# Performance work log

Hardware: AMD Instinct MI355X
Metric: run time of the kernel (lower is better)

## Reference

```python
import jax, jax.numpy as jnp
import numpy as np

N_NODES = 100000
N_RELS = 4
N_EDGES = 200000
D_IN = 256
D_OUT = 256
N_BASES = 2
LN_EPS = 1e-5


def setup_inputs() -> dict:
    key = jax.random.key(0)
    ks = jax.random.split(key, 8)
    x = jax.random.normal(ks[0], (N_NODES, D_IN), dtype=jnp.float32)
    src_idx = jax.random.randint(ks[1], (N_RELS, N_EDGES), 0, N_NODES, dtype=jnp.int32)
    dst_idx = jax.random.randint(ks[2], (N_RELS, N_EDGES), 0, N_NODES, dtype=jnp.int32)
    # WeightBasis: bases [B, in, out], per-relation coefficients [R, B]
    xav = float(np.sqrt(2.0)) * float(np.sqrt(6.0 / (D_IN + D_OUT)))
    bases = jax.random.uniform(ks[3], (N_BASES, D_IN, D_OUT), minval=-xav, maxval=xav, dtype=jnp.float32)
    w_comp = jax.random.normal(ks[4], (N_RELS, N_BASES), dtype=jnp.float32) * 0.5
    loop_weight = jax.random.uniform(ks[5], (D_IN, D_OUT), minval=-xav, maxval=xav, dtype=jnp.float32)
    h_bias = jnp.zeros((D_OUT,), dtype=jnp.float32)
    ln_gamma = jnp.ones((D_OUT,), dtype=jnp.float32)
    ln_beta = jnp.zeros((D_OUT,), dtype=jnp.float32)
    return {"x": x, "src_idx": src_idx, "dst_idx": dst_idx, "bases": bases,
            "w_comp": w_comp, "loop_weight": loop_weight, "h_bias": h_bias,
            "ln_gamma": ln_gamma, "ln_beta": ln_beta}


def reference(x, src_idx, dst_idx, bases, w_comp, loop_weight, h_bias, ln_gamma, ln_beta):
    n = x.shape[0]
    # basis combination -> per-relation weights [R, in, out]
    W = jnp.einsum('rb,bio->rio', w_comp, bases)

    def per_rel(W_r, s, d):
        # GraphConv(norm='right', weight=W_r): aggregate src feats to dst,
        # normalize by in-degree (clamped to 1), then matmul.
        msgs = x[s]                                            # [E, in]
        agg = jax.ops.segment_sum(msgs, d, num_segments=n)     # [N, in]
        deg = jax.ops.segment_sum(jnp.ones(d.shape, x.dtype), d, num_segments=n)
        agg = agg / jnp.maximum(deg, 1.0)[:, None]
        return agg @ W_r                                        # [N, out]

    hs = jax.vmap(per_rel)(W, src_idx, dst_idx).sum(axis=0)    # HeteroGraphConv sum aggregate
    # self-loop + bias
    h = hs + x @ loop_weight + h_bias
    # layer norm
    mu = jnp.mean(h, axis=-1, keepdims=True)
    var = jnp.mean(jnp.square(h - mu), axis=-1, keepdims=True)
    h = (h - mu) * jax.lax.rsqrt(var + LN_EPS) * ln_gamma + ln_beta
    # activation (dropout inactive in eval; NGNN has 0 layers)
    return jax.nn.relu(h)
```

## Files before the change

kernel.cpp:

```cpp
#include <hip/hip_runtime.h>


#define NN 100000
#define NR 4
#define NE 200000
#define BM 128

typedef __attribute__((ext_vector_type(8))) short short8;
typedef __attribute__((ext_vector_type(16))) float floatx16;

__device__ __forceinline__ unsigned short f2bf(float f) {
  unsigned u = __float_as_uint(f);
  u += 0x7FFFu + ((u >> 16) & 1u);
  return (unsigned short)(u >> 16);
}

__device__ __forceinline__ void gload16(const unsigned short* g, unsigned short* l) {
  __builtin_amdgcn_global_load_lds(
      (const __attribute__((address_space(1))) unsigned int*)g,
      (__attribute__((address_space(3))) unsigned int*)l, 16, 0, 0);
}

__global__ void prep(const float* __restrict__ x, const float* __restrict__ bases,
                     const float* __restrict__ loop_w, const int* __restrict__ src,
                     const int* __restrict__ dst, unsigned short* __restrict__ Xbf,
                     unsigned short* __restrict__ Bfrag, int* __restrict__ rec,
                     int* __restrict__ ovf) {
  const int b = blockIdx.x;
  const int tid = threadIdx.x;
  if (b < 3125) {
    int i = b * 256 + tid;
    int r = i / NE;
    int s = __builtin_nontemporal_load(src + i);
    int dd = __builtin_nontemporal_load(dst + i);
    int pos = atomicAdd(&rec[dd * 16], 1);
    int v = s | (r << 20);
    if (pos < 15) rec[dd * 16 + 1 + pos] = v;
    else if (pos < 31) ovf[dd * 16 + (pos - 15)] = v;
  } else if (b < 3893) {
    int i = (b - 3125) * 256 + tid;
    int e = i & 7;
    int lane = (i >> 3) & 63;
    int f = i >> 9;
    int t = f & 7;
    int j = (f >> 3) & 7;
    int s = f >> 6;
    int n = t * 32 + (lane & 31);
    int k = s * 128 + j * 16 + (lane >> 5) * 8 + e;
    float v;
    if (k < 256)      v = bases[k * 256 + n];
    else if (k < 512) v = bases[65536 + (k - 256) * 256 + n];
    else              v = loop_w[(k - 512) * 256 + n];
    Bfrag[i] = f2bf(v);
  } else {
    int i = (b - 3893) * 256 + tid;
    int row = i >> 5;
    int col = (i & 31) << 3;
    const float4 v0 = *(const float4*)(x + (size_t)row * 256 + col);
    const float4 v1 = *(const float4*)(x + (size_t)row * 256 + col + 4);
    uint4 u;
    u.x = (unsigned)f2bf(v0.x) | ((unsigned)f2bf(v0.y) << 16);
    u.y = (unsigned)f2bf(v0.z) | ((unsigned)f2bf(v0.w) << 16);
    u.z = (unsigned)f2bf(v1.x) | ((unsigned)f2bf(v1.y) << 16);
    u.w = (unsigned)f2bf(v1.z) | ((unsigned)f2bf(v1.w) << 16);
    *(uint4*)(Xbf + (size_t)row * 256 + col) = u;
  }
}

__global__ void agg_edges(const int* __restrict__ rec, const int* __restrict__ ovf,
                          const float* __restrict__ w_comp,
                          const unsigned short* __restrict__ Xbf,
                          unsigned short* __restrict__ A2) {
  const int tid = threadIdx.x;
  const int lane = tid & 63;
  const int wave = tid >> 6;
  const int half = lane >> 5;
  const int l31 = lane & 31;
  const int d = blockIdx.x * 8 + wave * 2 + half;
  const int selbase = lane & 32;

  int raw = 0;
  if (l31 < 16) raw = rec[d * 16 + l31];
  int cc = __shfl(raw, selbase);
  cc = cc < 31 ? cc : 31;
  int ev = 0;
  const bool val = (l31 >= 1) && (l31 <= cc);
  if (val) {
    if (l31 < 16) ev = raw;
    else ev = ovf[d * 16 + (l31 - 16)];
  }
  const int rl = (ev >> 20) & 3;

  unsigned long long b0 = __ballot(val && rl == 0);
  unsigned long long b1 = __ballot(val && rl == 1);
  unsigned long long b2 = __ballot(val && rl == 2);
  unsigned long long b3 = __ballot(val && rl == 3);
  const int sh = half << 5;
  float i0 = 1.0f / fmaxf((float)__popc((unsigned)(b0 >> sh)), 1.0f);
  float i1 = 1.0f / fmaxf((float)__popc((unsigned)(b1 >> sh)), 1.0f);
  float i2 = 1.0f / fmaxf((float)__popc((unsigned)(b2 >> sh)), 1.0f);
  float i3 = 1.0f / fmaxf((float)__popc((unsigned)(b3 >> sh)), 1.0f);
  float s00 = w_comp[0] * i0, s10 = w_comp[1] * i0;
  float s01 = w_comp[2] * i1, s11 = w_comp[3] * i1;
  float s02 = w_comp[4] * i2, s12 = w_comp[5] * i2;
  float s03 = w_comp[6] * i3, s13 = w_comp[7] * i3;

  float a0[8] = {0.f, 0.f, 0.f, 0.f, 0.f, 0.f, 0.f, 0.f};
  float a1[8] = {0.f, 0.f, 0.f, 0.f, 0.f, 0.f, 0.f, 0.f};
  const unsigned short* Xp = Xbf + l31 * 8;

#define EDGE_W(v, w0, w1)                                            \
  int r_##w0 = ((v) >> 20) & 3;                                      \
  float w0 = r_##w0 < 2 ? (r_##w0 == 0 ? s00 : s01)                  \
                        : (r_##w0 == 2 ? s02 : s03);                 \
  float w1 = r_##w0 < 2 ? (r_##w0 == 0 ? s10 : s11)                  \
                        : (r_##w0 == 2 ? s12 : s13);

#define ACC8(g, w0, w1)                                              \
  {                                                                  \
    float e0 = __uint_as_float((g).x << 16);                         \
    float e1 = __uint_as_float((g).x & 0xFFFF0000u);                 \
    float e2 = __uint_as_float((g).y << 16);                         \
    float e3 = __uint_as_float((g).y & 0xFFFF0000u);                 \
    float e4 = __uint_as_float((g).z << 16);                         \
    float e5 = __uint_as_float((g).z & 0xFFFF0000u);                 \
    float e6 = __uint_as_float((g).w << 16);                         \
    float e7 = __uint_as_float((g).w & 0xFFFF0000u);                 \
    a0[0] += (w0) * e0; a0[1] += (w0) * e1; a0[2] += (w0) * e2;      \
    a0[3] += (w0) * e3; a0[4] += (w0) * e4; a0[5] += (w0) * e5;      \
    a0[6] += (w0) * e6; a0[7] += (w0) * e7;                          \
    a1[0] += (w1) * e0; a1[1] += (w1) * e1; a1[2] += (w1) * e2;      \
    a1[3] += (w1) * e3; a1[4] += (w1) * e4; a1[5] += (w1) * e5;      \
    a1[6] += (w1) * e6; a1[7] += (w1) * e7;                          \
  }

  int i = 0;
  for (; i + 4 <= cc; i += 4) {
    int v0 = __shfl(ev, selbase + 1 + i);
    int v1 = __shfl(ev, selbase + 2 + i);
    int v2 = __shfl(ev, selbase + 3 + i);
    int v3 = __shfl(ev, selbase + 4 + i);
    const uint4 g0 = *(const uint4*)(Xp + (size_t)(v0 & 0xFFFFF) * 256);
    const uint4 g1 = *(const uint4*)(Xp + (size_t)(v1 & 0xFFFFF) * 256);
    const uint4 g2 = *(const uint4*)(Xp + (size_t)(v2 & 0xFFFFF) * 256);
    const uint4 g3 = *(const uint4*)(Xp + (size_t)(v3 & 0xFFFFF) * 256);
    { EDGE_W(v0, w0a, w1a) ACC8(g0, w0a, w1a) }
    { EDGE_W(v1, w0b, w1b) ACC8(g1, w0b, w1b) }
    { EDGE_W(v2, w0c, w1c) ACC8(g2, w0c, w1c) }
    { EDGE_W(v3, w0d, w1d) ACC8(g3, w0d, w1d) }
  }
  for (; i < cc; ++i) {
    int v = __shfl(ev, selbase + 1 + i);
    const uint4 g = *(const uint4*)(Xp + (size_t)(v & 0xFFFFF) * 256);
    EDGE_W(v, w0, w1)
    ACC8(g, w0, w1)
  }

  uint4 o0, o1;
  o0.x = (unsigned)f2bf(a0[0]) | ((unsigned)f2bf(a0[1]) << 16);
  o0.y = (unsigned)f2bf(a0[2]) | ((unsigned)f2bf(a0[3]) << 16);
  o0.z = (unsigned)f2bf(a0[4]) | ((unsigned)f2bf(a0[5]) << 16);
  o0.w = (unsigned)f2bf(a0[6]) | ((unsigned)f2bf(a0[7]) << 16);
  o1.x = (unsigned)f2bf(a1[0]) | ((unsigned)f2bf(a1[1]) << 16);
  o1.y = (unsigned)f2bf(a1[2]) | ((unsigned)f2bf(a1[3]) << 16);
  o1.z = (unsigned)f2bf(a1[4]) | ((unsigned)f2bf(a1[5]) << 16);
  o1.w = (unsigned)f2bf(a1[6]) | ((unsigned)f2bf(a1[7]) << 16);

  {
    const int m = d >> 7;
    const int rin = d & 127;
    const int w = rin >> 5;
    const int lr = rin & 31;
    const int s0 = l31 >> 2;
    const int jj = (l31 >> 1) & 1;
    const int hh = l31 & 1;
    size_t base = (size_t)m * 16 * 4096 + (size_t)(w * 2 + jj) * 512 + (size_t)(hh * 32 + lr) * 8;
    *(uint4*)(A2 + base + (size_t)s0 * 4096) = o0;
    *(uint4*)(A2 + base + (size_t)(8 + s0) * 4096) = o1;
  }
}

__launch_bounds__(256, 2)
__global__ void gemm_ln(const unsigned short* __restrict__ A2,
                        const unsigned short* __restrict__ Xbf,
                        const unsigned short* __restrict__ Bfrag,
                        const float* __restrict__ h_bias, const float* __restrict__ gamma,
                        const float* __restrict__ beta, float* __restrict__ out) {
  __shared__ unsigned short Ab[2][128 * 32];
  __shared__ unsigned short Bb[2][256 * 32];
  const int tid = threadIdx.x;
  const int wave = tid >> 6;
  const int lane = tid & 63;
  const int l31 = lane & 31;
  const int half = lane >> 5;
  const int m0 = blockIdx.x * BM;

  floatx16 acc[8];
#pragma unroll
  for (int t = 0; t < 8; ++t)
#pragma unroll
    for (int r = 0; r < 16; ++r) acc[t][r] = 0.0f;

  int arow = m0 + 32 * wave + l31;
  if (arow >= NN) arow = NN - 1;
  const unsigned short* pA2 = A2 + (size_t)blockIdx.x * 16 * 4096 + (size_t)(wave * 2) * 512 + (size_t)lane * 8;
  const unsigned short* pX0 = Xbf + (size_t)arow * 256 + half * 8;
  const unsigned short* pX1 = pX0 + 16;
  const unsigned short* pB = Bfrag + tid * 8;

#define STAGE(s, buf)                                                     \
  {                                                                       \
    if ((s) < 16) {                                                       \
      const unsigned short* asrc = pA2 + (size_t)(s) * 4096;              \
      gload16(asrc,       &Ab[buf][(wave * 2 + 0) * 512] + lane * 8);     \
      gload16(asrc + 512, &Ab[buf][(wave * 2 + 1) * 512] + lane * 8);     \
    } else {                                                              \
      const int ks = (s) * 32 - 512;                                      \
      gload16(pX0 + ks, &Ab[buf][(wave * 2 + 0) * 512] + lane * 8);       \
      gload16(pX1 + ks, &Ab[buf][(wave * 2 + 1) * 512] + lane * 8);       \
    }                                                                     \
    const unsigned short* bsrc = pB + (size_t)(s) * 8192;                 \
    gload16(bsrc,        &Bb[buf][0]    + tid * 8);                       \
    gload16(bsrc + 2048, &Bb[buf][2048] + tid * 8);                       \
    gload16(bsrc + 4096, &Bb[buf][4096] + tid * 8);                       \
    gload16(bsrc + 6144, &Bb[buf][6144] + tid * 8);                       \
  }

  STAGE(0, 0)

  for (int s = 0; s < 24; ++s) {
    const int cur = s & 1;
    if (s < 23) {
      STAGE(s + 1, cur ^ 1)
      asm volatile("s_waitcnt vmcnt(6)" ::: "memory");
    } else {
      asm volatile("s_waitcnt vmcnt(0)" ::: "memory");
    }
    __builtin_amdgcn_sched_barrier(0);
    __builtin_amdgcn_s_barrier();
    __builtin_amdgcn_sched_barrier(0);
#pragma unroll
    for (int j = 0; j < 2; ++j) {
      short8 af = *(const short8*)(&Ab[cur][(wave * 2 + j) * 512] + lane * 8);
#pragma unroll
      for (int t = 0; t < 8; ++t) {
        short8 bfr = *(const short8*)(&Bb[cur][(j * 8 + t) * 512] + lane * 8);
        acc[t] = __builtin_amdgcn_mfma_f32_32x32x16_bf16(af, bfr, acc[t], 0, 0, 0);
      }
    }
    __builtin_amdgcn_sched_barrier(0);
    __builtin_amdgcn_s_barrier();
    __builtin_amdgcn_sched_barrier(0);
  }

  float bcol[8], gc[8], bc[8];
#pragma unroll
  for (int t = 0; t < 8; ++t) {
    int col = t * 32 + l31;
    bcol[t] = h_bias[col];
    gc[t] = gamma[col];
    bc[t] = beta[col];
  }
#pragma unroll
  for (int t = 0; t < 8; ++t)
#pragma unroll
    for (int r = 0; r < 16; ++r) acc[t][r] += bcol[t];

  const int m_base = m0 + wave * 32;
#pragma unroll
  for (int r = 0; r < 16; ++r) {
    float s = 0.f, q = 0.f;
#pragma unroll
    for (int t = 0; t < 8; ++t) { float v = acc[t][r]; s += v; q += v * v; }
#pragma unroll
    for (int m = 16; m >= 1; m >>= 1) {
      s += __shfl_xor(s, m);
      q += __shfl_xor(q, m);
    }
    float mean = s * (1.0f / 256.0f);
    float var = q * (1.0f / 256.0f) - mean * mean;
    float rstd = rsqrtf(var + 1e-5f);
    int row = (r & 3) + ((r >> 2) << 3) + (half << 2);
    int grow = m_base + row;
    if (grow < NN) {
#pragma unroll
      for (int t = 0; t < 8; ++t) {
        float v = (acc[t][r] - mean) * rstd * gc[t] + bc[t];
        out[(size_t)grow * 256 + t * 32 + l31] = fmaxf(v, 0.0f);
      }
    }
  }
}

extern "C" void kernel_launch(void* const* d_in, const int* in_sizes, int n_in,
                              void* d_out, int out_size, void* d_ws, size_t ws_size,
                              hipStream_t stream) {
  const float* x      = (const float*)d_in[0];
  const int*   src    = (const int*)d_in[1];
  const int*   dst    = (const int*)d_in[2];
  const float* bases  = (const float*)d_in[3];
  const float* w_comp = (const float*)d_in[4];
  const float* loop_w = (const float*)d_in[5];
  const float* h_bias = (const float*)d_in[6];
  const float* gamma  = (const float*)d_in[7];
  const float* beta   = (const float*)d_in[8];
  float* out = (float*)d_out;

  char* ws = (char*)d_ws;
  unsigned short* A2    = (unsigned short*)ws;
  unsigned short* Xbf   = (unsigned short*)(ws + 102498304);
  unsigned short* Bfrag = (unsigned short*)(ws + 153698304);
  int* rec = (int*)(ws + 154091520);
  int* ovf = (int*)(ws + 160491520);

  hipMemsetAsync(rec, 0, 6400000, stream);

  prep<<<16393, 256, 0, stream>>>(x, bases, loop_w, src, dst, Xbf, Bfrag, rec, ovf);
  agg_edges<<<12500, 256, 0, stream>>>(rec, ovf, w_comp, Xbf, A2);
  gemm_ln<<<(NN + BM - 1) / BM, 256, 0, stream>>>(A2, Xbf, Bfrag, h_bias, gamma, beta, out);
}
```

Before: 389.2 us.

## Halve GEMM row tile to 64 and split output columns across wave pairs

Shrinks the fused GEMM+LayerNorm tile from 128 to 64 rows per block, giving 1563 blocks instead of 782 for better CU occupancy and load balance. Each wave now computes a 32x128 quarter instead of a 32x256 strip. LayerNorm row statistics are combined across wave pairs through a small shared-memory exchange. The A2 fragment layout written by the aggregation kernel and the workspace offsets are changed to match. B tiles are now reloaded per 64 rows, which doubles B traffic relative to A, and the extra sync adds a little overhead.

```diff
diff --git a/kernel.cpp b/kernel.cpp
--- a/kernel.cpp
+++ b/kernel.cpp
@@ -4,7 +4,8 @@
 #define NN 100000
 #define NR 4
 #define NE 200000
-#define BM 128
+#define BM 64
+#define NT 1563
 
 typedef __attribute__((ext_vector_type(8))) short short8;
 typedef __attribute__((ext_vector_type(16))) float floatx16;
@@ -167,16 +168,16 @@
   o1.w = (unsigned)f2bf(a1[6]) | ((unsigned)f2bf(a1[7]) << 16);
 
   {
-    const int m = d >> 7;
-    const int rin = d & 127;
-    const int w = rin >> 5;
+    const int m = d >> 6;
+    const int rin = d & 63;
+    const int rb = rin >> 5;
     const int lr = rin & 31;
     const int s0 = l31 >> 2;
     const int jj = (l31 >> 1) & 1;
     const int hh = l31 & 1;
-    size_t base = (size_t)m * 16 * 4096 + (size_t)(w * 2 + jj) * 512 + (size_t)(hh * 32 + lr) * 8;
-    *(uint4*)(A2 + base + (size_t)s0 * 4096) = o0;
-    *(uint4*)(A2 + base + (size_t)(8 + s0) * 4096) = o1;
+    size_t base = (size_t)m * 16 * 2048 + (size_t)((rb * 2 + jj) * 64 + hh * 32 + lr) * 8;
+    *(uint4*)(A2 + base + (size_t)s0 * 2048) = o0;
+    *(uint4*)(A2 + base + (size_t)(8 + s0) * 2048) = o1;
   }
 }
 
@@ -186,39 +187,34 @@
                         const unsigned short* __restrict__ Bfrag,
                         const float* __restrict__ h_bias, const float* __restrict__ gamma,
                         const float* __restrict__ beta, float* __restrict__ out) {
-  __shared__ unsigned short Ab[2][128 * 32];
+  __shared__ unsigned short Ab[2][64 * 32];
   __shared__ unsigned short Bb[2][256 * 32];
+  __shared__ float LNx[4][2][16][2];
   const int tid = threadIdx.x;
   const int wave = tid >> 6;
   const int lane = tid & 63;
   const int l31 = lane & 31;
   const int half = lane >> 5;
+  const int rb = wave & 1;
+  const int nh = wave >> 1;
   const int m0 = blockIdx.x * BM;
 
-  floatx16 acc[8];
-#pragma unroll
-  for (int t = 0; t < 8; ++t)
+  floatx16 acc[4];
+#pragma unroll
+  for (int t = 0; t < 4; ++t)
 #pragma unroll
     for (int r = 0; r < 16; ++r) acc[t][r] = 0.0f;
 
-  int arow = m0 + 32 * wave + l31;
-  if (arow >= NN) arow = NN - 1;
-  const unsigned short* pA2 = A2 + (size_t)blockIdx.x * 16 * 4096 + (size_t)(wave * 2) * 512 + (size_t)lane * 8;
-  const unsigned short* pX0 = Xbf + (size_t)arow * 256 + half * 8;
-  const unsigned short* pX1 = pX0 + 16;
+  const unsigned short* pA2 = A2 + (size_t)blockIdx.x * 16 * 2048 + (size_t)tid * 8;
+  int xr = m0 + (tid >> 7) * 32 + (tid & 31);
+  if (xr >= NN) xr = NN - 1;
+  const unsigned short* pX = Xbf + (size_t)xr * 256 + ((tid >> 6) & 1) * 16 + ((tid >> 5) & 1) * 8;
   const unsigned short* pB = Bfrag + tid * 8;
 
 #define STAGE(s, buf)                                                     \
   {                                                                       \
-    if ((s) < 16) {                                                       \
-      const unsigned short* asrc = pA2 + (size_t)(s) * 4096;              \
-      gload16(asrc,       &Ab[buf][(wave * 2 + 0) * 512] + lane * 8);     \
-      gload16(asrc + 512, &Ab[buf][(wave * 2 + 1) * 512] + lane * 8);     \
-    } else {                                                              \
-      const int ks = (s) * 32 - 512;                                      \
-      gload16(pX0 + ks, &Ab[buf][(wave * 2 + 0) * 512] + lane * 8);       \
-      gload16(pX1 + ks, &Ab[buf][(wave * 2 + 1) * 512] + lane * 8);       \
-    }                                                                     \
+    if ((s) < 16) gload16(pA2 + (size_t)(s) * 2048, &Ab[buf][0] + tid * 8); \
+    else          gload16(pX + (s) * 32 - 512,      &Ab[buf][0] + tid * 8); \
     const unsigned short* bsrc = pB + (size_t)(s) * 8192;                 \
     gload16(bsrc,        &Bb[buf][0]    + tid * 8);                       \
     gload16(bsrc + 2048, &Bb[buf][2048] + tid * 8);                       \
@@ -232,7 +228,7 @@
     const int cur = s & 1;
     if (s < 23) {
       STAGE(s + 1, cur ^ 1)
-      asm volatile("s_waitcnt vmcnt(6)" ::: "memory");
+      asm volatile("s_waitcnt vmcnt(5)" ::: "memory");
     } else {
       asm volatile("s_waitcnt vmcnt(0)" ::: "memory");
     }
@@ -241,10 +237,10 @@
     __builtin_amdgcn_sched_barrier(0);
 #pragma unroll
     for (int j = 0; j < 2; ++j) {
-      short8 af = *(const short8*)(&Ab[cur][(wave * 2 + j) * 512] + lane * 8);
-#pragma unroll
-      for (int t = 0; t < 8; ++t) {
-        short8 bfr = *(const short8*)(&Bb[cur][(j * 8 + t) * 512] + lane * 8);
+      short8 af = *(const short8*)(&Ab[cur][((rb * 2 + j) * 64 + lane) * 8]);
+#pragma unroll
+      for (int t = 0; t < 4; ++t) {
+        short8 bfr = *(const short8*)(&Bb[cur][(j * 8 + nh * 4 + t) * 512 + lane * 8]);
         acc[t] = __builtin_amdgcn_mfma_f32_32x32x16_bf16(af, bfr, acc[t], 0, 0, 0);
       }
     }
@@ -253,40 +249,56 @@
     __builtin_amdgcn_sched_barrier(0);
   }
 
-  float bcol[8], gc[8], bc[8];
-#pragma unroll
-  for (int t = 0; t < 8; ++t) {
-    int col = t * 32 + l31;
+  float bcol[4], gc[4], bc[4];
+#pragma unroll
+  for (int t = 0; t < 4; ++t) {
+    int col = nh * 128 + t * 32 + l31;
     bcol[t] = h_bias[col];
     gc[t] = gamma[col];
     bc[t] = beta[col];
   }
 #pragma unroll
-  for (int t = 0; t < 8; ++t)
+  for (int t = 0; t < 4; ++t)
 #pragma unroll
     for (int r = 0; r < 16; ++r) acc[t][r] += bcol[t];
 
-  const int m_base = m0 + wave * 32;
 #pragma unroll
   for (int r = 0; r < 16; ++r) {
     float s = 0.f, q = 0.f;
 #pragma unroll
-    for (int t = 0; t < 8; ++t) { float v = acc[t][r]; s += v; q += v * v; }
+    for (int t = 0; t < 4; ++t) { float v = acc[t][r]; s += v; q += v * v; }
 #pragma unroll
     for (int m = 16; m >= 1; m >>= 1) {
       s += __shfl_xor(s, m);
       q += __shfl_xor(q, m);
     }
-    float mean = s * (1.0f / 256.0f);
-    float var = q * (1.0f / 256.0f) - mean * mean;
+    if (l31 == 0) { LNx[wave][half][r][0] = s; LNx[wave][half][r][1] = q; }
+  }
+  __syncthreads();
+
+  const int m_base = m0 + rb * 32;
+#pragma unroll
+  for (int r = 0; r < 16; ++r) {
+    float s = 0.f, q = 0.f;
+#pragma unroll
+    for (int t = 0; t < 4; ++t) { float v = acc[t][r]; s += v; q += v * v; }
+#pragma unroll
+    for (int m = 16; m >= 1; m >>= 1) {
+      s += __shfl_xor(s, m);
+      q += __shfl_xor(q, m);
+    }
+    float S = s + LNx[wave ^ 2][half][r][0];
+    float Q = q + LNx[wave ^ 2][half][r][1];
+    float mean = S * (1.0f / 256.0f);
+    float var = Q * (1.0f / 256.0f) - mean * mean;
     float rstd = rsqrtf(var + 1e-5f);
     int row = (r & 3) + ((r >> 2) << 3) + (half << 2);
     int grow = m_base + row;
     if (grow < NN) {
 #pragma unroll
-      for (int t = 0; t < 8; ++t) {
+      for (int t = 0; t < 4; ++t) {
         float v = (acc[t][r] - mean) * rstd * gc[t] + bc[t];
-        out[(size_t)grow * 256 + t * 32 + l31] = fmaxf(v, 0.0f);
+        out[(size_t)grow * 256 + nh * 128 + t * 32 + l31] = fmaxf(v, 0.0f);
       }
     }
   }
@@ -308,14 +320,14 @@
 
   char* ws = (char*)d_ws;
   unsigned short* A2    = (unsigned short*)ws;
-  unsigned short* Xbf   = (unsigned short*)(ws + 102498304);
-  unsigned short* Bfrag = (unsigned short*)(ws + 153698304);
-  int* rec = (int*)(ws + 154091520);
-  int* ovf = (int*)(ws + 160491520);
+  unsigned short* Xbf   = (unsigned short*)(ws + 102432768);
+  unsigned short* Bfrag = (unsigned short*)(ws + 153632768);
+  int* rec = (int*)(ws + 154025984);
+  int* ovf = (int*)(ws + 160425984);
 
   hipMemsetAsync(rec, 0, 6400000, stream);
 
   prep<<<16393, 256, 0, stream>>>(x, bases, loop_w, src, dst, Xbf, Bfrag, rec, ovf);
   agg_edges<<<12500, 256, 0, stream>>>(rec, ovf, w_comp, Xbf, A2);
-  gemm_ln<<<(NN + BM - 1) / BM, 256, 0, stream>>>(A2, Xbf, Bfrag, h_bias, gamma, beta, out);
-}
+  gemm_ln<<<NT, 256, 0, stream>>>(A2, Xbf, Bfrag, h_bias, gamma, beta, out);
+}
```

New measurement: 406.7 us. 4.5% more time.
